# Kernel tuning notes

Measured on AMD Instinct MI355X. Metric: run time of the kernel, lower is better.

The kernel has to match this reference:

```python
import jax, jax.numpy as jnp
import numpy as np

IN_F, OUT_F = 128, 128
B, N = 4, 4096

def setup_inputs() -> dict:
    key = jax.random.key(0)
    k1, k2, k3 = jax.random.split(key, 3)
    relation_matrix = jax.random.uniform(k1, (B, N, N), dtype=jnp.float32)
    inputs = jax.random.normal(k2, (B, N, IN_F), dtype=jnp.float32)
    w = jax.random.normal(k3, (IN_F, OUT_F), dtype=jnp.float32)
    return {"relation_matrix": relation_matrix, "inputs": inputs, "w": w}

def reference(relation_matrix, inputs, w):
    # deg_i = sum_j A_ij ; D = diag(deg) + I  -> inverse is elementwise reciprocal
    deg = jnp.sum(relation_matrix, axis=-1) + 1.0            # [B, N]
    # (A + I) @ X  == A @ X + X  (avoids materializing A + eye)
    ax = jnp.einsum('bnm,bmf->bnf', relation_matrix, inputs) + inputs  # [B, N, in]
    z = (ax / deg[..., None]) @ w                            # [B, N, out]
    return jax.nn.relu(z)
```

## Files before the change

kernel.cpp:

```cpp
#include <hip/hip_runtime.h>
#include <hip/hip_bf16.h>
#include <stdint.h>

#define NN 4096
#define NF 128
#define NB 4

typedef __attribute__((ext_vector_type(4))) float  floatx4;
typedef __attribute__((ext_vector_type(8))) __bf16 bf16x8;

__global__ __launch_bounds__(256) void prep_kernel(const float* __restrict__ X,
                                                   const float* __restrict__ w,
                                                   __bf16* __restrict__ Xpack,
                                                   __bf16* __restrict__ wpack) {
    const int tid = threadIdx.x;
    const int bx  = blockIdx.x;
    if (bx == 256) {
        for (int p = tid; p < 512; p += 256) {
            int kc = p >> 7, n = p & 127;
#pragma unroll
            for (int k8 = 0; k8 < 32; k8 += 8) {
                bf16x8 v;
#pragma unroll
                for (int j = 0; j < 8; j++)
                    v[j] = (__bf16)w[(size_t)(kc * 32 + k8 + j) * NF + n];
                *(bf16x8*)(wpack + ((size_t)(kc * 128 + n)) * 32 + k8) = v;
            }
        }
        return;
    }
    int id = bx * 256 + tid;
    int b  = id >> 14;
    int kc = (id >> 7) & 127;
    int n  = id & 127;
    const float* Xp = X + ((size_t)b * NN + (size_t)kc * 32) * NF + n;
    __bf16* op = Xpack + (((size_t)b * 128 + kc) * 128 + n) * 32;
#pragma unroll
    for (int k8 = 0; k8 < 32; k8 += 8) {
        bf16x8 v;
#pragma unroll
        for (int j = 0; j < 8; j++)
            v[j] = (__bf16)Xp[(size_t)(k8 + j) * NF];
        *(bf16x8*)(op + k8) = v;
    }
}

__global__ __launch_bounds__(256, 4) void main_kernel(const float* __restrict__ A,
                                                      const float* __restrict__ X,
                                                      const __bf16* __restrict__ Xpack,
                                                      const __bf16* __restrict__ wpack,
                                                      float* __restrict__ out) {
    __shared__ __bf16 Us[16][136];

    const int tid  = threadIdx.x;
    const int wv   = tid >> 6;
    const int lane = tid & 63;
    const int lm   = lane & 15;
    const int quad = lane >> 4;

    const int b  = blockIdx.x >> 8;
    const int m0 = (blockIdx.x & 255) << 4;

    const float*  Arow = A + ((size_t)b * NN + m0 + lm) * NN + quad * 8;
    const __bf16* Bp   = Xpack + ((size_t)b * 128 * NF + (wv * 32 + lm)) * 32 + quad * 8;

    floatx4 acc0 = {0.f, 0.f, 0.f, 0.f};
    floatx4 acc1 = {0.f, 0.f, 0.f, 0.f};
    float dsum = 0.f;

    floatx4 a0 = *(const floatx4*)(Arow);
    floatx4 a1 = *(const floatx4*)(Arow + 4);
    bf16x8  b0 = *(const bf16x8*)(Bp);
    bf16x8  b1 = *(const bf16x8*)(Bp + 512);

#pragma unroll 4
    for (int kc = 0; kc < 127; kc++) {
        const float*  An = Arow + (size_t)(kc + 1) * 32;
        const __bf16* Bn = Bp + (size_t)(kc + 1) * 4096;
        floatx4 na0 = *(const floatx4*)(An);
        floatx4 na1 = *(const floatx4*)(An + 4);
        bf16x8  nb0 = *(const bf16x8*)(Bn);
        bf16x8  nb1 = *(const bf16x8*)(Bn + 512);

        dsum += a0[0] + a0[1] + a0[2] + a0[3] + a1[0] + a1[1] + a1[2] + a1[3];
        bf16x8 af;
#pragma unroll
        for (int i = 0; i < 4; i++) af[i] = (__bf16)a0[i];
#pragma unroll
        for (int i = 0; i < 4; i++) af[4 + i] = (__bf16)a1[i];
        acc0 = __builtin_amdgcn_mfma_f32_16x16x32_bf16(af, b0, acc0, 0, 0, 0);
        acc1 = __builtin_amdgcn_mfma_f32_16x16x32_bf16(af, b1, acc1, 0, 0, 0);

        a0 = na0; a1 = na1; b0 = nb0; b1 = nb1;
    }
    {
        dsum += a0[0] + a0[1] + a0[2] + a0[3] + a1[0] + a1[1] + a1[2] + a1[3];
        bf16x8 af;
#pragma unroll
        for (int i = 0; i < 4; i++) af[i] = (__bf16)a0[i];
#pragma unroll
        for (int i = 0; i < 4; i++) af[4 + i] = (__bf16)a1[i];
        acc0 = __builtin_amdgcn_mfma_f32_16x16x32_bf16(af, b0, acc0, 0, 0, 0);
        acc1 = __builtin_amdgcn_mfma_f32_16x16x32_bf16(af, b1, acc1, 0, 0, 0);
    }

    dsum += __shfl_xor(dsum, 16, 64);
    dsum += __shfl_xor(dsum, 32, 64);
    float degv[4];
#pragma unroll
    for (int i = 0; i < 4; i++)
        degv[i] = __shfl(dsum, quad * 4 + i, 64) + 1.0f;

    bf16x8 wf[4][2];
#pragma unroll
    for (int kc2 = 0; kc2 < 4; kc2++)
#pragma unroll
        for (int nt = 0; nt < 2; nt++)
            wf[kc2][nt] = *(const bf16x8*)(wpack +
                ((size_t)(kc2 * 128 + wv * 32 + nt * 16 + lm)) * 32 + quad * 8);

    const float* Xb = X + ((size_t)b * NN + m0) * NF;
#pragma unroll
    for (int nt = 0; nt < 2; nt++) {
        int col = wv * 32 + nt * 16 + lm;
        floatx4 accv = nt ? acc1 : acc0;
#pragma unroll
        for (int i = 0; i < 4; i++) {
            int r = quad * 4 + i;
            float u = (accv[i] + Xb[(size_t)r * NF + col]) / degv[i];
            Us[r][col] = (__bf16)u;
        }
    }
    __syncthreads();

    floatx4 z0 = {0.f, 0.f, 0.f, 0.f};
    floatx4 z1 = {0.f, 0.f, 0.f, 0.f};
#pragma unroll
    for (int kc2 = 0; kc2 < 4; kc2++) {
        bf16x8 ua = *(const bf16x8*)&Us[lm][kc2 * 32 + quad * 8];
        z0 = __builtin_amdgcn_mfma_f32_16x16x32_bf16(ua, wf[kc2][0], z0, 0, 0, 0);
        z1 = __builtin_amdgcn_mfma_f32_16x16x32_bf16(ua, wf[kc2][1], z1, 0, 0, 0);
    }

    float* ob = out + ((size_t)b * NN + m0) * NF;
#pragma unroll
    for (int nt = 0; nt < 2; nt++) {
        int col = wv * 32 + nt * 16 + lm;
        floatx4 zv = nt ? z1 : z0;
#pragma unroll
        for (int i = 0; i < 4; i++) {
            int r = quad * 4 + i;
            float v = zv[i];
            ob[(size_t)r * NF + col] = v > 0.f ? v : 0.f;
        }
    }
}

extern "C" void kernel_launch(void* const* d_in, const int* in_sizes, int n_in,
                              void* d_out, int out_size, void* d_ws, size_t ws_size,
                              hipStream_t stream) {
    const float* A = (const float*)d_in[0];
    const float* X = (const float*)d_in[1];
    const float* w = (const float*)d_in[2];
    float* out = (float*)d_out;

    __bf16* Xpack = (__bf16*)d_ws;
    __bf16* wpack = Xpack + (size_t)NB * NF * NN;

    prep_kernel<<<257, 256, 0, stream>>>(X, w, Xpack, wpack);
    main_kernel<<<1024, 256, 0, stream>>>(A, X, Xpack, wpack, out);
}
```

Measured before the change: 471.6 us.

## Stage A tiles through LDS with async global_load_lds double buffering

The main kernel now streams 16x256 tiles of the fp32 relation matrix into a double-buffered LDS array using global_load_lds. Each wavefront loads whole contiguous rows, giving coalesced 1 KB accesses, where previously each lane issued strided 32-byte register loads per row. The prep kernel also transposes X through a shared-memory tile so reads are coalesced, and it now uses 512 blocks. In exchange the main kernel takes on about 33 KB of LDS, a barrier per stage and a manual waitcnt encoding, which may cut occupancy and adds correctness risk in the stage synchronisation.

Result: faster. 399.2 us (-15.4%).

```diff
diff --git a/kernel.cpp b/kernel.cpp
--- a/kernel.cpp
+++ b/kernel.cpp
@@ -5,17 +5,26 @@
 #define NN 4096
 #define NF 128
 #define NB 4
+#define KC 256
+#define NSTAGE (NN / KC)
 
 typedef __attribute__((ext_vector_type(4))) float  floatx4;
 typedef __attribute__((ext_vector_type(8))) __bf16 bf16x8;
+
+__device__ __forceinline__ void load_lds_16(const float* g, float* l) {
+    __builtin_amdgcn_global_load_lds(
+        (const __attribute__((address_space(1))) uint32_t*)g,
+        (__attribute__((address_space(3))) uint32_t*)l, 16, 0, 0);
+}
 
 __global__ __launch_bounds__(256) void prep_kernel(const float* __restrict__ X,
                                                    const float* __restrict__ w,
                                                    __bf16* __restrict__ Xpack,
                                                    __bf16* __restrict__ wpack) {
+    __shared__ float Xs[32][129];
     const int tid = threadIdx.x;
     const int bx  = blockIdx.x;
-    if (bx == 256) {
+    if (bx == 512) {
         for (int p = tid; p < 512; p += 256) {
             int kc = p >> 7, n = p & 127;
 #pragma unroll
@@ -29,20 +38,25 @@
         }
         return;
     }
-    int id = bx * 256 + tid;
-    int b  = id >> 14;
-    int kc = (id >> 7) & 127;
-    int n  = id & 127;
-    const float* Xp = X + ((size_t)b * NN + (size_t)kc * 32) * NF + n;
-    __bf16* op = Xpack + (((size_t)b * 128 + kc) * 128 + n) * 32;
+    const int b  = bx >> 7;
+    const int kc = bx & 127;
+    const float* Xt = X + ((size_t)b * NN + (size_t)kc * 32) * NF;
 #pragma unroll
-    for (int k8 = 0; k8 < 32; k8 += 8) {
-        bf16x8 v;
+    for (int j = 0; j < 16; j++) {
+        int i = tid + j * 256;
+        Xs[i >> 7][i & 127] = Xt[i];
+    }
+    __syncthreads();
+    const int f  = tid >> 1;
+    const int kh = (tid & 1) * 16;
+    bf16x8 v0, v1;
 #pragma unroll
-        for (int j = 0; j < 8; j++)
-            v[j] = (__bf16)Xp[(size_t)(k8 + j) * NF];
-        *(bf16x8*)(op + k8) = v;
-    }
+    for (int j = 0; j < 8; j++) v0[j] = (__bf16)Xs[kh + j][f];
+#pragma unroll
+    for (int j = 0; j < 8; j++) v1[j] = (__bf16)Xs[kh + 8 + j][f];
+    __bf16* op = Xpack + (((size_t)b * 128 + kc) * 128 + f) * 32 + kh;
+    *(bf16x8*)op = v0;
+    *(bf16x8*)(op + 8) = v1;
 }
 
 __global__ __launch_bounds__(256, 4) void main_kernel(const float* __restrict__ A,
@@ -50,6 +64,7 @@
                                                       const __bf16* __restrict__ Xpack,
                                                       const __bf16* __restrict__ wpack,
                                                       float* __restrict__ out) {
+    __shared__ float  At[2][16][260];
     __shared__ __bf16 Us[16][136];
 
     const int tid  = threadIdx.x;
@@ -61,47 +76,46 @@
     const int b  = blockIdx.x >> 8;
     const int m0 = (blockIdx.x & 255) << 4;
 
-    const float*  Arow = A + ((size_t)b * NN + m0 + lm) * NN + quad * 8;
-    const __bf16* Bp   = Xpack + ((size_t)b * 128 * NF + (wv * 32 + lm)) * 32 + quad * 8;
+    const float* Ag[4];
+#pragma unroll
+    for (int j = 0; j < 4; j++)
+        Ag[j] = A + ((size_t)b * NN + m0 + wv * 4 + j) * NN + lane * 4;
+
+    const __bf16* Bbase = Xpack + ((size_t)b * 128 * NF + (wv * 32 + lm)) * 32 + quad * 8;
 
     floatx4 acc0 = {0.f, 0.f, 0.f, 0.f};
     floatx4 acc1 = {0.f, 0.f, 0.f, 0.f};
     float dsum = 0.f;
 
-    floatx4 a0 = *(const floatx4*)(Arow);
-    floatx4 a1 = *(const floatx4*)(Arow + 4);
-    bf16x8  b0 = *(const bf16x8*)(Bp);
-    bf16x8  b1 = *(const bf16x8*)(Bp + 512);
+#pragma unroll
+    for (int j = 0; j < 4; j++)
+        load_lds_16(Ag[j], &At[0][wv * 4 + j][0]);
 
-#pragma unroll 4
-    for (int kc = 0; kc < 127; kc++) {
-        const float*  An = Arow + (size_t)(kc + 1) * 32;
-        const __bf16* Bn = Bp + (size_t)(kc + 1) * 4096;
-        floatx4 na0 = *(const floatx4*)(An);
-        floatx4 na1 = *(const floatx4*)(An + 4);
-        bf16x8  nb0 = *(const bf16x8*)(Bn);
-        bf16x8  nb1 = *(const bf16x8*)(Bn + 512);
-
-        dsum += a0[0] + a0[1] + a0[2] + a0[3] + a1[0] + a1[1] + a1[2] + a1[3];
-        bf16x8 af;
+    for (int s = 0; s < NSTAGE; s++) {
+        const int buf = s & 1;
+        __builtin_amdgcn_s_waitcnt(0x0f70);
+        __syncthreads();
+        if (s + 1 < NSTAGE) {
 #pragma unroll
-        for (int i = 0; i < 4; i++) af[i] = (__bf16)a0[i];
+            for (int j = 0; j < 4; j++)
+                load_lds_16(Ag[j] + (size_t)(s + 1) * KC, &At[buf ^ 1][wv * 4 + j][0]);
+        }
+        const __bf16* Bs = Bbase + (size_t)s * 8 * 4096;
 #pragma unroll
-        for (int i = 0; i < 4; i++) af[4 + i] = (__bf16)a1[i];
-        acc0 = __builtin_amdgcn_mfma_f32_16x16x32_bf16(af, b0, acc0, 0, 0, 0);
-        acc1 = __builtin_amdgcn_mfma_f32_16x16x32_bf16(af, b1, acc1, 0, 0, 0);
-
-        a0 = na0; a1 = na1; b0 = nb0; b1 = nb1;
-    }
-    {
-        dsum += a0[0] + a0[1] + a0[2] + a0[3] + a1[0] + a1[1] + a1[2] + a1[3];
-        bf16x8 af;
+        for (int kk = 0; kk < 8; kk++) {
+            bf16x8 b0 = *(const bf16x8*)(Bs + (size_t)kk * 4096);
+            bf16x8 b1 = *(const bf16x8*)(Bs + (size_t)kk * 4096 + 512);
+            floatx4 a0 = *(const floatx4*)&At[buf][lm][kk * 32 + quad * 8];
+            floatx4 a1 = *(const floatx4*)&At[buf][lm][kk * 32 + quad * 8 + 4];
+            dsum += a0[0] + a0[1] + a0[2] + a0[3] + a1[0] + a1[1] + a1[2] + a1[3];
+            bf16x8 af;
 #pragma unroll
-        for (int i = 0; i < 4; i++) af[i] = (__bf16)a0[i];
+            for (int i = 0; i < 4; i++) af[i] = (__bf16)a0[i];
 #pragma unroll
-        for (int i = 0; i < 4; i++) af[4 + i] = (__bf16)a1[i];
-        acc0 = __builtin_amdgcn_mfma_f32_16x16x32_bf16(af, b0, acc0, 0, 0, 0);
-        acc1 = __builtin_amdgcn_mfma_f32_16x16x32_bf16(af, b1, acc1, 0, 0, 0);
+            for (int i = 0; i < 4; i++) af[4 + i] = (__bf16)a1[i];
+            acc0 = __builtin_amdgcn_mfma_f32_16x16x32_bf16(af, b0, acc0, 0, 0, 0);
+            acc1 = __builtin_amdgcn_mfma_f32_16x16x32_bf16(af, b1, acc1, 0, 0, 0);
+        }
     }
 
     dsum += __shfl_xor(dsum, 16, 64);
@@ -167,6 +181,6 @@
     __bf16* Xpack = (__bf16*)d_ws;
     __bf16* wpack = Xpack + (size_t)NB * NF * NN;
 
-    prep_kernel<<<257, 256, 0, stream>>>(X, w, Xpack, wpack);
+    prep_kernel<<<513, 256, 0, stream>>>(X, w, Xpack, wpack);
     main_kernel<<<1024, 256, 0, stream>>>(A, X, Xpack, wpack, out);
 }
```
